# Performance work log

Hardware: AMD Instinct MI355X
Metric: run time of the kernel (lower is better)

The kernel has to match this reference:

```python
import jax, jax.numpy as jnp
import numpy as np

NB, NG = 100000, 20000   # bus / gen node counts
D, H = 64, 64            # input feat dim, hidden dim
EL, EX = 1000000, 200000 # line edges, gen<->bus edges
OUT = 16


def setup_inputs() -> dict:
    key = jax.random.key(0)
    ks = jax.random.split(key, 28)

    def nrm(k, shp, scale):
        return jax.random.normal(k, shp, jnp.float32) * scale

    w = 0.05  # small weight scale to keep activations tame over stacked layers
    inp = {
        "x_bus": nrm(ks[0], (NB, D), 1.0),
        "x_gen": nrm(ks[1], (NG, D), 1.0),
        "line_src": jax.random.randint(ks[2], (EL,), 0, NB, jnp.int32),
        "line_dst": jax.random.randint(ks[3], (EL,), 0, NB, jnp.int32),
        "g2b_src": jax.random.randint(ks[4], (EX,), 0, NG, jnp.int32),
        "g2b_dst": jax.random.randint(ks[5], (EX,), 0, NB, jnp.int32),
        "b2g_src": jax.random.randint(ks[6], (EX,), 0, NB, jnp.int32),
        "b2g_dst": jax.random.randint(ks[7], (EX,), 0, NG, jnp.int32),
    }
    i = 8
    for l in range(2):
        din = D if l == 0 else H
        for name in ["W_self_bus", "W_self_gen", "W_line", "W_g2b", "W_b2g"]:
            inp[f"{name}_{l}"] = nrm(ks[i], (din, H), w); i += 1
        inp[f"b_self_bus_{l}"] = jnp.zeros((H,), jnp.float32)
        inp[f"b_self_gen_{l}"] = jnp.zeros((H,), jnp.float32)
    inp["W_h"] = nrm(ks[i], (2 * H, H), w); i += 1
    inp["b_h"] = jnp.zeros((H,), jnp.float32)
    inp["W_o"] = nrm(ks[i], (H, OUT), w); i += 1
    inp["b_o"] = jnp.zeros((OUT,), jnp.float32)
    return inp


def _mean_aggr(msg_src, src, dst, n_dst):
    # transform-at-source already applied; gather then mean-scatter to dst nodes
    m = msg_src[src]  # [E, H]
    s = jax.ops.segment_sum(m, dst, num_segments=n_dst)
    c = jax.ops.segment_sum(jnp.ones(dst.shape, m.dtype), dst, num_segments=n_dst)
    return s / jnp.maximum(c, 1.0)[:, None]


def reference(x_bus, x_gen, line_src, line_dst, g2b_src, g2b_dst, b2g_src, b2g_dst,
              W_self_bus_0, W_self_gen_0, W_line_0, W_g2b_0, W_b2g_0,
              b_self_bus_0, b_self_gen_0,
              W_self_bus_1, W_self_gen_1, W_line_1, W_g2b_1, W_b2g_1,
              b_self_bus_1, b_self_gen_1,
              W_h, b_h, W_o, b_o):
    layers = [
        (W_self_bus_0, b_self_bus_0, W_self_gen_0, b_self_gen_0, W_line_0, W_g2b_0, W_b2g_0),
        (W_self_bus_1, b_self_bus_1, W_self_gen_1, b_self_gen_1, W_line_1, W_g2b_1, W_b2g_1),
    ]
    hb, hg = x_bus, x_gen
    nb, ng = hb.shape[0], hg.shape[0]
    for (Wsb, bsb, Wsg, bsg, Wl, Wg2b, Wb2g) in layers:
        m_line = _mean_aggr(hb @ Wl, line_src, line_dst, nb)   # bus -> bus
        m_g2b = _mean_aggr(hg @ Wg2b, g2b_src, g2b_dst, nb)    # gen -> bus
        m_b2g = _mean_aggr(hb @ Wb2g, b2g_src, b2g_dst, ng)    # bus -> gen
        new_hb = jax.nn.relu(hb @ Wsb + bsb + m_line + m_g2b)
        new_hg = jax.nn.relu(hg @ Wsg + bsg + m_b2g)
        hb, hg = new_hb, new_hg
    # sum-pool each node type, concat, 2-layer MLP head
    g = jnp.concatenate([jnp.sum(hb, axis=0), jnp.sum(hg, axis=0)], axis=-1)
    return jax.nn.relu(g @ W_h + b_h) @ W_o + b_o
```

## Files before the change

### kernel.cpp

```cpp
#include <hip/hip_runtime.h>

#define NB 100000
#define NG 20000
#define EL 1000000
#define EX 200000
#define NSEG (2 * NB + NG)
#define NE (EL + 2 * EX)
#define WROW 72
#define WMAT (64 * WROW)
#define AST 200
#define FPB 128
#define PSEG (NSEG / 8)
#define CAPL 40
#define CAPG 16
#define CAPB 40
#define FILL_BLOCKS (8 * FPB)
#define PB_W 10
#define PB_CB (NB * 64 / 1024)
#define PB_CG (NG * 64 / 1024)
#define BUILD_TOTAL (FILL_BLOCKS + PB_W + PB_CB + PB_CG + 1)

typedef __attribute__((ext_vector_type(8))) short bf16x8;
typedef __attribute__((ext_vector_type(4))) float f32x4;

static __device__ __forceinline__ int uni(int x) { return __builtin_amdgcn_readfirstlane(x); }

static __device__ __forceinline__ unsigned short f2bf(float x) {
    unsigned u = __float_as_uint(x);
    u += 0x7FFF + ((u >> 16) & 1);
    return (unsigned short)(u >> 16);
}
static __device__ __forceinline__ float bf2f(unsigned short s) {
    return __uint_as_float(((unsigned)s) << 16);
}

struct WPrep { const float* src[10]; unsigned short* dst[10]; };
__global__ __launch_bounds__(256) void build_kernel(
    WPrep wp, const float* __restrict__ xb, const float* __restrict__ xg,
    unsigned short* __restrict__ xb16, unsigned short* __restrict__ xg16,
    const int* __restrict__ ls, const int* __restrict__ ld,
    const int* __restrict__ gs, const int* __restrict__ gd,
    const int* __restrict__ bs, const int* __restrict__ bd,
    int* __restrict__ cnt, int* __restrict__ bktL,
    int* __restrict__ bktG, int* __restrict__ bktB,
    float* __restrict__ pool)
{
    const int b = blockIdx.x;
    const int t = threadIdx.x;
    if (b < FILL_BLOCKS) {
        const int p = b & 7;
        const int q = b >> 3;
        const int lo = p * PSEG;
        const int hi = lo + PSEG;
        for (int i = q * 256 + t; i < NE; i += FPB * 256) {
            int src, seg, cap;
            int* dst;
            if (i < EL) {
                src = ls[i]; int d = ld[i];
                seg = d; dst = bktL + (size_t)d * CAPL; cap = CAPL;
            } else if (i < EL + EX) {
                src = gs[i - EL]; int d = gd[i - EL];
                seg = NB + d; dst = bktG + (size_t)d * CAPG; cap = CAPG;
            } else {
                src = bs[i - EL - EX]; int d = bd[i - EL - EX];
                seg = 2 * NB + d; dst = bktB + (size_t)d * CAPB; cap = CAPB;
            }
            if (seg >= lo && seg < hi) {
                int pos = atomicAdd(&cnt[seg], 1);
                if (pos < cap) dst[pos] = src;
            }
        }
    } else if (b < FILL_BLOCKS + PB_W) {
        const float* __restrict__ s = wp.src[b - FILL_BLOCKS];
        unsigned short* __restrict__ d = wp.dst[b - FILL_BLOCKS];
        for (int idx = t; idx < 4096; idx += 256) {
            int k = idx >> 6, nn = idx & 63;
            d[nn * WROW + k] = f2bf(s[idx]);
        }
    } else if (b < FILL_BLOCKS + PB_W + PB_CB) {
        int i = ((b - FILL_BLOCKS - PB_W) * 256 + t) * 4;
        float4 f = *(const float4*)(xb + i);
        ushort4 u = { f2bf(f.x), f2bf(f.y), f2bf(f.z), f2bf(f.w) };
        *(ushort4*)(xb16 + i) = u;
    } else if (b < FILL_BLOCKS + PB_W + PB_CB + PB_CG) {
        int i = ((b - FILL_BLOCKS - PB_W - PB_CB) * 256 + t) * 4;
        float4 f = *(const float4*)(xg + i);
        ushort4 u = { f2bf(f.x), f2bf(f.y), f2bf(f.z), f2bf(f.w) };
        *(ushort4*)(xg16 + i) = u;
    } else {
        if (t < 128) pool[t] = 0.f;
    }
}

static __device__ __forceinline__ float seg_mean_lds(const unsigned short* __restrict__ h,
                                                     const int* ib,
                                                     int c, int cap, int lane) {
    float s = 0.f;
    const int n = min(c, cap);
    int e = 0;
    for (; e + 8 <= n; e += 8) {
        int i0 = ib[e],     i1 = ib[e + 1], i2 = ib[e + 2], i3 = ib[e + 3];
        int i4 = ib[e + 4], i5 = ib[e + 5], i6 = ib[e + 6], i7 = ib[e + 7];
        float v0 = bf2f(h[(size_t)i0 * 64 + lane]), v1 = bf2f(h[(size_t)i1 * 64 + lane]);
        float v2 = bf2f(h[(size_t)i2 * 64 + lane]), v3 = bf2f(h[(size_t)i3 * 64 + lane]);
        float v4 = bf2f(h[(size_t)i4 * 64 + lane]), v5 = bf2f(h[(size_t)i5 * 64 + lane]);
        float v6 = bf2f(h[(size_t)i6 * 64 + lane]), v7 = bf2f(h[(size_t)i7 * 64 + lane]);
        s += ((v0 + v1) + (v2 + v3)) + ((v4 + v5) + (v6 + v7));
    }
    for (; e + 2 <= n; e += 2) {
        int i0 = ib[e], i1 = ib[e + 1];
        s += bf2f(h[(size_t)i0 * 64 + lane]) + bf2f(h[(size_t)i1 * 64 + lane]);
    }
    if (e < n) s += bf2f(h[(size_t)ib[e] * 64 + lane]);
    return s / fmaxf((float)c, 1.f);
}

__global__ __launch_bounds__(256) void combine_fused_kernel(
    const unsigned short* __restrict__ hb, const unsigned short* __restrict__ hg,
    const int* __restrict__ cnt,
    const int* __restrict__ bktL, const int* __restrict__ bktG, const int* __restrict__ bktB,
    const unsigned short* __restrict__ WtB, const unsigned short* __restrict__ WtG,
    const float* __restrict__ biasB, const float* __restrict__ biasG,
    unsigned short* __restrict__ outB, unsigned short* __restrict__ outG,
    float* __restrict__ pool, int gbBus)
{
    __shared__ __attribute__((aligned(16))) unsigned short Atile[32 * AST];
    __shared__ int ibuf[32 * (CAPL + CAPG)];
    __shared__ int cbuf[64];
    __shared__ float pred[64];
    const int t = threadIdx.x;
    const bool isBus = blockIdx.x < gbBus;
    const int bb = isBus ? blockIdx.x : blockIdx.x - gbBus;
    const int base = bb * 32;
    const int nmat = isBus ? 3 : 2;
    const unsigned short* __restrict__ h = isBus ? hb : hg;
    const unsigned short* __restrict__ Wt = isBus ? WtB : WtG;
    const float* __restrict__ bias = isBus ? biasB : biasG;

    if (pool != nullptr && t < 64) pred[t] = 0.f;

#pragma unroll
    for (int i = 0; i < 2; ++i) {
        int flat = i * 1024 + t * 4;
        int r = flat >> 6, c = flat & 63;
        *(ushort4*)&Atile[r * AST + c] = *(const ushort4*)(h + (size_t)(base + r) * 64 + c);
    }

    if (isBus) {
        for (int i = t; i < 32 * CAPL; i += 256) ibuf[i] = bktL[(size_t)base * CAPL + i];
        for (int i = t; i < 32 * CAPG; i += 256) ibuf[32 * CAPL + i] = bktG[(size_t)base * CAPG + i];
        if (t < 32) { cbuf[t] = cnt[base + t]; cbuf[32 + t] = cnt[NB + base + t]; }
    } else {
        for (int i = t; i < 32 * CAPB; i += 256) ibuf[i] = bktB[(size_t)base * CAPB + i];
        if (t < 32) cbuf[t] = cnt[2 * NB + base + t];
    }
    __syncthreads();

    const int lane = t & 63;
    const int w = t >> 6;
    for (int r8 = 0; r8 < 8; ++r8) {
        const int r = w * 8 + r8;
        if (isBus) {
            int cA = uni(cbuf[r]);
            float vA = seg_mean_lds(hb, &ibuf[r * CAPL], cA, CAPL, lane);
            Atile[r * AST + 64 + lane] = f2bf(vA);
            int cB = uni(cbuf[32 + r]);
            float vB = seg_mean_lds(hg, &ibuf[32 * CAPL + r * CAPG], cB, CAPG, lane);
            Atile[r * AST + 128 + lane] = f2bf(vB);
        } else {
            int cA = uni(cbuf[r]);
            float vA = seg_mean_lds(hb, &ibuf[r * CAPB], cA, CAPB, lane);
            Atile[r * AST + 64 + lane] = f2bf(vA);
        }
    }
    __syncthreads();

    const int rg = w & 1;
    const int cp = w >> 1;
    const int l15 = lane & 15;
    const int q = lane >> 4;
    f32x4 acc[2];
    acc[0] = (f32x4){0.f, 0.f, 0.f, 0.f};
    acc[1] = (f32x4){0.f, 0.f, 0.f, 0.f};

    const int ksteps = nmat * 2;
    for (int ks = 0; ks < ksteps; ++ks) {
        bf16x8 av = *(const bf16x8*)&Atile[(rg * 16 + l15) * AST + ks * 32 + q * 8];
#pragma unroll
        for (int cc = 0; cc < 2; ++cc) {
            int c = cp * 2 + cc;
            bf16x8 bv = *(const bf16x8*)&Wt[(ks >> 1) * WMAT + (c * 16 + l15) * WROW + (ks & 1) * 32 + q * 8];
            acc[cc] = __builtin_amdgcn_mfma_f32_16x16x32_bf16(av, bv, acc[cc], 0, 0, 0);
        }
    }

    if (pool == nullptr) {
        unsigned short* __restrict__ out = isBus ? outB : outG;
#pragma unroll
        for (int cc = 0; cc < 2; ++cc) {
            const int col = (cp * 2 + cc) * 16 + l15;
            const float bv = bias[col];
#pragma unroll
            for (int reg = 0; reg < 4; ++reg) {
                int row = base + rg * 16 + q * 4 + reg;
                out[(size_t)row * 64 + col] = f2bf(fmaxf(acc[cc][reg] + bv, 0.f));
            }
        }
    } else {
        float* __restrict__ pdst = isBus ? pool : pool + 64;
#pragma unroll
        for (int cc = 0; cc < 2; ++cc) {
            const int col = (cp * 2 + cc) * 16 + l15;
            const float bv = bias[col];
            float s = 0.f;
#pragma unroll
            for (int reg = 0; reg < 4; ++reg) {
                s += fmaxf(acc[cc][reg] + bv, 0.f);
            }
            atomicAdd(&pred[col], s);
        }
        __syncthreads();
        if (t < 64) atomicAdd(&pdst[t], pred[t]);
    }
}

__global__ void head_kernel(const float* __restrict__ pool,
                            const float* __restrict__ Wh, const float* __restrict__ bh,
                            const float* __restrict__ Wo, const float* __restrict__ bo,
                            float* __restrict__ out)
{
    __shared__ float g[128];
    __shared__ float hid[64];
    int t = threadIdx.x;
    g[t] = pool[t];
    __syncthreads();
    if (t < 64) {
        float a = bh[t];
        for (int i = 0; i < 128; ++i) a += g[i] * Wh[i * 64 + t];
        hid[t] = fmaxf(a, 0.f);
    }
    __syncthreads();
    if (t < 16) {
        float a = bo[t];
        for (int j = 0; j < 64; ++j) a += hid[j] * Wo[j * 16 + t];
        out[t] = a;
    }
}

extern "C" void kernel_launch(void* const* d_in, const int* in_sizes, int n_in,
                              void* d_out, int out_size, void* d_ws, size_t ws_size,
                              hipStream_t stream)
{
    const float* x_bus   = (const float*)d_in[0];
    const float* x_gen   = (const float*)d_in[1];
    const int* line_src  = (const int*)d_in[2];
    const int* line_dst  = (const int*)d_in[3];
    const int* g2b_src   = (const int*)d_in[4];
    const int* g2b_dst   = (const int*)d_in[5];
    const int* b2g_src   = (const int*)d_in[6];
    const int* b2g_dst   = (const int*)d_in[7];
    const float* Wsb[2]  = {(const float*)d_in[8],  (const float*)d_in[15]};
    const float* Wsg[2]  = {(const float*)d_in[9],  (const float*)d_in[16]};
    const float* Wl[2]   = {(const float*)d_in[10], (const float*)d_in[17]};
    const float* Wg2b[2] = {(const float*)d_in[11], (const float*)d_in[18]};
    const float* Wb2g[2] = {(const float*)d_in[12], (const float*)d_in[19]};
    const float* bsb[2]  = {(const float*)d_in[13], (const float*)d_in[20]};
    const float* bsg[2]  = {(const float*)d_in[14], (const float*)d_in[21]};
    const float* Wh = (const float*)d_in[22];
    const float* bh = (const float*)d_in[23];
    const float* Wo = (const float*)d_in[24];
    const float* bo = (const float*)d_in[25];
    (void)in_sizes; (void)n_in; (void)out_size; (void)ws_size;

    char* wsB = (char*)d_ws;
    size_t o = 0;
    auto alloc_f = [&](size_t nelem) { o = (o + 15) & ~(size_t)15; float* p = (float*)(wsB + o); o += nelem * sizeof(float); return p; };
    auto alloc_i = [&](size_t nelem) { o = (o + 15) & ~(size_t)15; int* p = (int*)(wsB + o); o += nelem * sizeof(int); return p; };
    auto alloc_u = [&](size_t nelem) { o = (o + 15) & ~(size_t)15; unsigned short* p = (unsigned short*)(wsB + o); o += nelem * sizeof(unsigned short); return p; };

    unsigned short* xb16  = alloc_u((size_t)NB * 64);
    unsigned short* xg16  = alloc_u((size_t)NG * 64);
    unsigned short* H1b   = alloc_u((size_t)NB * 64);
    unsigned short* H1g   = alloc_u((size_t)NG * 64);
    int*   bktL = alloc_i((size_t)NB * CAPL);
    int*   bktG = alloc_i((size_t)NB * CAPG);
    int*   bktB = alloc_i((size_t)NG * CAPB);
    int*   cnt  = alloc_i(NSEG);
    float* pool = alloc_f(128);
    unsigned short* WtBus[2] = { alloc_u(3 * WMAT), alloc_u(3 * WMAT) };
    unsigned short* WtGen[2] = { alloc_u(2 * WMAT), alloc_u(2 * WMAT) };

    hipMemsetAsync(cnt, 0, NSEG * sizeof(int), stream);
    WPrep wp;
    for (int l = 0; l < 2; ++l) {
        wp.src[l * 5 + 0] = Wsb[l];  wp.dst[l * 5 + 0] = WtBus[l] + 0 * WMAT;
        wp.src[l * 5 + 1] = Wl[l];   wp.dst[l * 5 + 1] = WtBus[l] + 1 * WMAT;
        wp.src[l * 5 + 2] = Wg2b[l]; wp.dst[l * 5 + 2] = WtBus[l] + 2 * WMAT;
        wp.src[l * 5 + 3] = Wsg[l];  wp.dst[l * 5 + 3] = WtGen[l] + 0 * WMAT;
        wp.src[l * 5 + 4] = Wb2g[l]; wp.dst[l * 5 + 4] = WtGen[l] + 1 * WMAT;
    }
    build_kernel<<<BUILD_TOTAL, 256, 0, stream>>>(
        wp, x_bus, x_gen, xb16, xg16,
        line_src, line_dst, g2b_src, g2b_dst, b2g_src, b2g_dst,
        cnt, bktL, bktG, bktB, pool);

    const int gbBus = NB / 32;
    const int gbGen = NG / 32;

    combine_fused_kernel<<<gbBus + gbGen, 256, 0, stream>>>(
        xb16, xg16, cnt, bktL, bktG, bktB, WtBus[0], WtGen[0], bsb[0], bsg[0],
        H1b, H1g, nullptr, gbBus);

    combine_fused_kernel<<<gbBus + gbGen, 256, 0, stream>>>(
        H1b, H1g, cnt, bktL, bktG, bktB, WtBus[1], WtGen[1], bsb[1], bsg[1],
        nullptr, nullptr, pool, gbBus);

    head_kernel<<<1, 128, 0, stream>>>(pool, Wh, bh, Wo, bo, (float*)d_out);
}
```

Baseline: 315.3 us.

## Interleave paired-row gathers and fuse head MLP via last-block completion counter

The mean-aggregation loop now processes two destination rows together, issuing sixteen independent gather loads per iteration so more memory requests are in flight per wave. The separate head kernel is removed. Instead, each block of the second layer increments a global completion counter, and the last block to finish reads the pooled sums and computes the MLP head. This saves one kernel launch but adds an atomic and threadfence per block, plus higher register pressure in the paired gather loop.

```diff
diff --git a/kernel.cpp b/kernel.cpp
--- a/kernel.cpp
+++ b/kernel.cpp
@@ -43,7 +43,7 @@
     const int* __restrict__ bs, const int* __restrict__ bd,
     int* __restrict__ cnt, int* __restrict__ bktL,
     int* __restrict__ bktG, int* __restrict__ bktB,
-    float* __restrict__ pool)
+    float* __restrict__ pool, int* __restrict__ done)
 {
     const int b = blockIdx.x;
     const int t = threadIdx.x;
@@ -89,30 +89,65 @@
         *(ushort4*)(xg16 + i) = u;
     } else {
         if (t < 128) pool[t] = 0.f;
-    }
-}
-
-static __device__ __forceinline__ float seg_mean_lds(const unsigned short* __restrict__ h,
-                                                     const int* ib,
-                                                     int c, int cap, int lane) {
-    float s = 0.f;
-    const int n = min(c, cap);
-    int e = 0;
-    for (; e + 8 <= n; e += 8) {
-        int i0 = ib[e],     i1 = ib[e + 1], i2 = ib[e + 2], i3 = ib[e + 3];
-        int i4 = ib[e + 4], i5 = ib[e + 5], i6 = ib[e + 6], i7 = ib[e + 7];
-        float v0 = bf2f(h[(size_t)i0 * 64 + lane]), v1 = bf2f(h[(size_t)i1 * 64 + lane]);
-        float v2 = bf2f(h[(size_t)i2 * 64 + lane]), v3 = bf2f(h[(size_t)i3 * 64 + lane]);
-        float v4 = bf2f(h[(size_t)i4 * 64 + lane]), v5 = bf2f(h[(size_t)i5 * 64 + lane]);
-        float v6 = bf2f(h[(size_t)i6 * 64 + lane]), v7 = bf2f(h[(size_t)i7 * 64 + lane]);
-        s += ((v0 + v1) + (v2 + v3)) + ((v4 + v5) + (v6 + v7));
-    }
-    for (; e + 2 <= n; e += 2) {
-        int i0 = ib[e], i1 = ib[e + 1];
-        s += bf2f(h[(size_t)i0 * 64 + lane]) + bf2f(h[(size_t)i1 * 64 + lane]);
-    }
-    if (e < n) s += bf2f(h[(size_t)ib[e] * 64 + lane]);
-    return s / fmaxf((float)c, 1.f);
+        if (t == 128) *done = 0;
+    }
+}
+
+static __device__ __forceinline__ void seg_mean_pair(
+    const unsigned short* __restrict__ h,
+    const int* ib0, int c0, const int* ib1, int c1, int cap, int lane,
+    float* __restrict__ m0, float* __restrict__ m1)
+{
+    float s0 = 0.f, s1 = 0.f;
+    const int n0 = min(c0, cap), n1 = min(c1, cap);
+    int e0 = 0, e1 = 0;
+    while (e0 + 8 <= n0 && e1 + 8 <= n1) {
+        int a0 = ib0[e0],     a1 = ib0[e0 + 1], a2 = ib0[e0 + 2], a3 = ib0[e0 + 3];
+        int a4 = ib0[e0 + 4], a5 = ib0[e0 + 5], a6 = ib0[e0 + 6], a7 = ib0[e0 + 7];
+        int b0 = ib1[e1],     b1 = ib1[e1 + 1], b2 = ib1[e1 + 2], b3 = ib1[e1 + 3];
+        int b4 = ib1[e1 + 4], b5 = ib1[e1 + 5], b6 = ib1[e1 + 6], b7 = ib1[e1 + 7];
+        float x0 = bf2f(h[(size_t)a0 * 64 + lane]), x1 = bf2f(h[(size_t)a1 * 64 + lane]);
+        float x2 = bf2f(h[(size_t)a2 * 64 + lane]), x3 = bf2f(h[(size_t)a3 * 64 + lane]);
+        float x4 = bf2f(h[(size_t)a4 * 64 + lane]), x5 = bf2f(h[(size_t)a5 * 64 + lane]);
+        float x6 = bf2f(h[(size_t)a6 * 64 + lane]), x7 = bf2f(h[(size_t)a7 * 64 + lane]);
+        float y0 = bf2f(h[(size_t)b0 * 64 + lane]), y1 = bf2f(h[(size_t)b1 * 64 + lane]);
+        float y2 = bf2f(h[(size_t)b2 * 64 + lane]), y3 = bf2f(h[(size_t)b3 * 64 + lane]);
+        float y4 = bf2f(h[(size_t)b4 * 64 + lane]), y5 = bf2f(h[(size_t)b5 * 64 + lane]);
+        float y6 = bf2f(h[(size_t)b6 * 64 + lane]), y7 = bf2f(h[(size_t)b7 * 64 + lane]);
+        s0 += ((x0 + x1) + (x2 + x3)) + ((x4 + x5) + (x6 + x7));
+        s1 += ((y0 + y1) + (y2 + y3)) + ((y4 + y5) + (y6 + y7));
+        e0 += 8; e1 += 8;
+    }
+    for (; e0 + 8 <= n0; e0 += 8) {
+        int a0 = ib0[e0],     a1 = ib0[e0 + 1], a2 = ib0[e0 + 2], a3 = ib0[e0 + 3];
+        int a4 = ib0[e0 + 4], a5 = ib0[e0 + 5], a6 = ib0[e0 + 6], a7 = ib0[e0 + 7];
+        float x0 = bf2f(h[(size_t)a0 * 64 + lane]), x1 = bf2f(h[(size_t)a1 * 64 + lane]);
+        float x2 = bf2f(h[(size_t)a2 * 64 + lane]), x3 = bf2f(h[(size_t)a3 * 64 + lane]);
+        float x4 = bf2f(h[(size_t)a4 * 64 + lane]), x5 = bf2f(h[(size_t)a5 * 64 + lane]);
+        float x6 = bf2f(h[(size_t)a6 * 64 + lane]), x7 = bf2f(h[(size_t)a7 * 64 + lane]);
+        s0 += ((x0 + x1) + (x2 + x3)) + ((x4 + x5) + (x6 + x7));
+    }
+    for (; e1 + 8 <= n1; e1 += 8) {
+        int b0 = ib1[e1],     b1 = ib1[e1 + 1], b2 = ib1[e1 + 2], b3 = ib1[e1 + 3];
+        int b4 = ib1[e1 + 4], b5 = ib1[e1 + 5], b6 = ib1[e1 + 6], b7 = ib1[e1 + 7];
+        float y0 = bf2f(h[(size_t)b0 * 64 + lane]), y1 = bf2f(h[(size_t)b1 * 64 + lane]);
+        float y2 = bf2f(h[(size_t)b2 * 64 + lane]), y3 = bf2f(h[(size_t)b3 * 64 + lane]);
+        float y4 = bf2f(h[(size_t)b4 * 64 + lane]), y5 = bf2f(h[(size_t)b5 * 64 + lane]);
+        float y6 = bf2f(h[(size_t)b6 * 64 + lane]), y7 = bf2f(h[(size_t)b7 * 64 + lane]);
+        s1 += ((y0 + y1) + (y2 + y3)) + ((y4 + y5) + (y6 + y7));
+    }
+    for (; e0 + 2 <= n0; e0 += 2) {
+        int i0 = ib0[e0], i1 = ib0[e0 + 1];
+        s0 += bf2f(h[(size_t)i0 * 64 + lane]) + bf2f(h[(size_t)i1 * 64 + lane]);
+    }
+    if (e0 < n0) s0 += bf2f(h[(size_t)ib0[e0] * 64 + lane]);
+    for (; e1 + 2 <= n1; e1 += 2) {
+        int i0 = ib1[e1], i1 = ib1[e1 + 1];
+        s1 += bf2f(h[(size_t)i0 * 64 + lane]) + bf2f(h[(size_t)i1 * 64 + lane]);
+    }
+    if (e1 < n1) s1 += bf2f(h[(size_t)ib1[e1] * 64 + lane]);
+    *m0 = s0 / fmaxf((float)c0, 1.f);
+    *m1 = s1 / fmaxf((float)c1, 1.f);
 }
 
 __global__ __launch_bounds__(256) void combine_fused_kernel(
@@ -122,12 +157,16 @@
     const unsigned short* __restrict__ WtB, const unsigned short* __restrict__ WtG,
     const float* __restrict__ biasB, const float* __restrict__ biasG,
     unsigned short* __restrict__ outB, unsigned short* __restrict__ outG,
-    float* __restrict__ pool, int gbBus)
+    float* __restrict__ pool, int gbBus,
+    const float* __restrict__ Wh, const float* __restrict__ bh,
+    const float* __restrict__ Wo, const float* __restrict__ bo,
+    float* __restrict__ outHead, int* __restrict__ done)
 {
     __shared__ __attribute__((aligned(16))) unsigned short Atile[32 * AST];
     __shared__ int ibuf[32 * (CAPL + CAPG)];
     __shared__ int cbuf[64];
     __shared__ float pred[64];
+    __shared__ int lastFlag;
     const int t = threadIdx.x;
     const bool isBus = blockIdx.x < gbBus;
     const int bb = isBus ? blockIdx.x : blockIdx.x - gbBus;
@@ -158,19 +197,26 @@
 
     const int lane = t & 63;
     const int w = t >> 6;
-    for (int r8 = 0; r8 < 8; ++r8) {
-        const int r = w * 8 + r8;
+#pragma unroll
+    for (int j = 0; j < 4; ++j) {
+        const int r0 = w * 8 + 2 * j;
+        const int r1 = r0 + 1;
+        float mA0, mA1;
         if (isBus) {
-            int cA = uni(cbuf[r]);
-            float vA = seg_mean_lds(hb, &ibuf[r * CAPL], cA, CAPL, lane);
-            Atile[r * AST + 64 + lane] = f2bf(vA);
-            int cB = uni(cbuf[32 + r]);
-            float vB = seg_mean_lds(hg, &ibuf[32 * CAPL + r * CAPG], cB, CAPG, lane);
-            Atile[r * AST + 128 + lane] = f2bf(vB);
+            seg_mean_pair(hb, &ibuf[r0 * CAPL], uni(cbuf[r0]),
+                          &ibuf[r1 * CAPL], uni(cbuf[r1]), CAPL, lane, &mA0, &mA1);
+            float mB0, mB1;
+            seg_mean_pair(hg, &ibuf[32 * CAPL + r0 * CAPG], uni(cbuf[32 + r0]),
+                          &ibuf[32 * CAPL + r1 * CAPG], uni(cbuf[32 + r1]), CAPG, lane, &mB0, &mB1);
+            Atile[r0 * AST + 64 + lane] = f2bf(mA0);
+            Atile[r1 * AST + 64 + lane] = f2bf(mA1);
+            Atile[r0 * AST + 128 + lane] = f2bf(mB0);
+            Atile[r1 * AST + 128 + lane] = f2bf(mB1);
         } else {
-            int cA = uni(cbuf[r]);
-            float vA = seg_mean_lds(hb, &ibuf[r * CAPB], cA, CAPB, lane);
-            Atile[r * AST + 64 + lane] = f2bf(vA);
+            seg_mean_pair(hb, &ibuf[r0 * CAPB], uni(cbuf[r0]),
+                          &ibuf[r1 * CAPB], uni(cbuf[r1]), CAPB, lane, &mA0, &mA1);
+            Atile[r0 * AST + 64 + lane] = f2bf(mA0);
+            Atile[r1 * AST + 64 + lane] = f2bf(mA1);
         }
     }
     __syncthreads();
@@ -221,29 +267,30 @@
         }
         __syncthreads();
         if (t < 64) atomicAdd(&pdst[t], pred[t]);
-    }
-}
-
-__global__ void head_kernel(const float* __restrict__ pool,
-                            const float* __restrict__ Wh, const float* __restrict__ bh,
-                            const float* __restrict__ Wo, const float* __restrict__ bo,
-                            float* __restrict__ out)
-{
-    __shared__ float g[128];
-    __shared__ float hid[64];
-    int t = threadIdx.x;
-    g[t] = pool[t];
-    __syncthreads();
-    if (t < 64) {
-        float a = bh[t];
-        for (int i = 0; i < 128; ++i) a += g[i] * Wh[i * 64 + t];
-        hid[t] = fmaxf(a, 0.f);
-    }
-    __syncthreads();
-    if (t < 16) {
-        float a = bo[t];
-        for (int j = 0; j < 64; ++j) a += hid[j] * Wo[j * 16 + t];
-        out[t] = a;
+
+        if (t == 0) {
+            __threadfence();
+            int r = atomicAdd(done, 1);
+            lastFlag = (r == (int)gridDim.x - 1) ? 1 : 0;
+        }
+        __syncthreads();
+        if (lastFlag) {
+            __shared__ float gbuf[128];
+            __shared__ float hid[64];
+            if (t < 128) gbuf[t] = atomicAdd(&pool[t], 0.f);
+            __syncthreads();
+            if (t < 64) {
+                float a = bh[t];
+                for (int i = 0; i < 128; ++i) a += gbuf[i] * Wh[i * 64 + t];
+                hid[t] = fmaxf(a, 0.f);
+            }
+            __syncthreads();
+            if (t < 16) {
+                float a = bo[t];
+                for (int jj = 0; jj < 64; ++jj) a += hid[jj] * Wo[jj * 16 + t];
+                outHead[t] = a;
+            }
+        }
     }
 }
 
@@ -286,6 +333,7 @@
     int*   bktG = alloc_i((size_t)NB * CAPG);
     int*   bktB = alloc_i((size_t)NG * CAPB);
     int*   cnt  = alloc_i(NSEG);
+    int*   done = alloc_i(4);
     float* pool = alloc_f(128);
     unsigned short* WtBus[2] = { alloc_u(3 * WMAT), alloc_u(3 * WMAT) };
     unsigned short* WtGen[2] = { alloc_u(2 * WMAT), alloc_u(2 * WMAT) };
@@ -302,18 +350,18 @@
     build_kernel<<<BUILD_TOTAL, 256, 0, stream>>>(
         wp, x_bus, x_gen, xb16, xg16,
         line_src, line_dst, g2b_src, g2b_dst, b2g_src, b2g_dst,
-        cnt, bktL, bktG, bktB, pool);
+        cnt, bktL, bktG, bktB, pool, done);
 
     const int gbBus = NB / 32;
     const int gbGen = NG / 32;
 
     combine_fused_kernel<<<gbBus + gbGen, 256, 0, stream>>>(
         xb16, xg16, cnt, bktL, bktG, bktB, WtBus[0], WtGen[0], bsb[0], bsg[0],
-        H1b, H1g, nullptr, gbBus);
+        H1b, H1g, nullptr, gbBus,
+        nullptr, nullptr, nullptr, nullptr, nullptr, nullptr);
 
     combine_fused_kernel<<<gbBus + gbGen, 256, 0, stream>>>(
         H1b, H1g, cnt, bktL, bktG, bktB, WtBus[1], WtGen[1], bsb[1], bsg[1],
-        nullptr, nullptr, pool, gbBus);
-
-    head_kernel<<<1, 128, 0, stream>>>(pool, Wh, bh, Wo, bo, (float*)d_out);
-}
+        nullptr, nullptr, pool, gbBus,
+        Wh, bh, Wo, bo, (float*)d_out, done);
+}
```

Result: slower. 423.1 us (+34.2%).
